# Optimization experiments

Hardware: AMD Instinct MI355X
Metric: run time of the kernel (lower is better)

The kernel has to match this reference:

```python
import jax, jax.numpy as jnp
import numpy as np

N = 50000
E = 800000
D = 128
NUM_GRAPHS = 64
NEG_SLOPE = 0.2


def _gat_conv(x, src, dst, W, a_src, a_dst, bias):
    """PyG GATConv with heads=1, concat=True. src/dst include self-loops."""
    h = x @ W                                  # [N, D_out]
    alpha_s = h @ a_src                        # [N]
    alpha_d = h @ a_dst                        # [N]
    e = alpha_s[src] + alpha_d[dst]            # [E_tot] edge scores
    e = jnp.where(e > 0, e, NEG_SLOPE * e)     # LeakyReLU(0.2)
    # numerically-stable softmax over incoming edges of each dst node
    m = jax.ops.segment_max(e, dst, num_segments=N)
    m = jnp.where(jnp.isfinite(m), m, 0.0)
    ex = jnp.exp(e - m[dst])
    s = jax.ops.segment_sum(ex, dst, num_segments=N)
    coef = ex / (s[dst] + 1e-16)               # [E_tot]
    msg = h[src] * coef[:, None]               # [E_tot, D_out] gathered messages
    out = jax.ops.segment_sum(msg, dst, num_segments=N)
    return out + bias


def setup_inputs() -> dict:
    key = jax.random.key(0)
    ks = jax.random.split(key, 12)
    x = jax.random.normal(ks[0], (N, D), dtype=jnp.float32)
    edge_index = jax.random.randint(ks[1], (2, E), 0, N, dtype=jnp.int64)
    batch = jnp.sort(jax.random.randint(ks[2], (N,), 0, NUM_GRAPHS, dtype=jnp.int64))
    g = 1.0 / np.sqrt(D)
    W1 = jax.random.normal(ks[3], (D, D), dtype=jnp.float32) * g
    as1 = jax.random.normal(ks[4], (D,), dtype=jnp.float32) * g
    ad1 = jax.random.normal(ks[5], (D,), dtype=jnp.float32) * g
    b1 = jnp.zeros((D,), dtype=jnp.float32)
    W2 = jax.random.normal(ks[6], (D, D), dtype=jnp.float32) * g
    as2 = jax.random.normal(ks[7], (D,), dtype=jnp.float32) * g
    ad2 = jax.random.normal(ks[8], (D,), dtype=jnp.float32) * g
    b2 = jnp.zeros((D,), dtype=jnp.float32)
    return {"x": x, "edge_index": edge_index, "batch": batch,
            "W1": W1, "as1": as1, "ad1": ad1, "b1": b1,
            "W2": W2, "as2": as2, "ad2": ad2, "b2": b2}


def reference(x, edge_index, batch, W1, as1, ad1, b1, W2, as2, ad2, b2):
    # PyG GATConv adds self-loops by default
    loops = jnp.arange(N, dtype=edge_index.dtype)
    src = jnp.concatenate([edge_index[0], loops])
    dst = jnp.concatenate([edge_index[1], loops])
    feats = _gat_conv(x, src, dst, W1, as1, ad1, b1)
    feats = _gat_conv(feats, src, dst, W2, as2, ad2, b2)
    # global mean pool over graphs in the batch
    sums = jax.ops.segment_sum(feats, batch, num_segments=NUM_GRAPHS)
    counts = jax.ops.segment_sum(jnp.ones((N,), feats.dtype), batch, num_segments=NUM_GRAPHS)
    pooled = sums / jnp.maximum(counts, 1.0)[:, None]
    return feats, pooled
```

## Files before the change

kernel.cpp:

```cpp
#include <hip/hip_runtime.h>

#define NN 50000
#define NE 800000
#define DIM 128
#define NG 64
#define ETOT (NE + NN)
#define NEG_SLOPE 0.2f
#define PB 200
#define MAXLG 8
#define NSH 8
#define SHW ((NN + NSH - 1) / NSH)
#define NB_SCAN ((NN + 255) / 256)

typedef unsigned int uint32;

static __device__ __forceinline__ uint32 f2bf_pack(float lo, float hi) {
  uint32 a = __float_as_uint(lo), b = __float_as_uint(hi);
  a = (a + 0x7fffu + ((a >> 16) & 1u)) >> 16;
  b = (b + 0x7fffu + ((b >> 16) & 1u)) >> 16;
  return a | (b << 16);
}
static __device__ __forceinline__ float bf_lo(uint32 u) { return __uint_as_float(u << 16); }
static __device__ __forceinline__ float bf_hi(uint32 u) { return __uint_as_float(u & 0xffff0000u); }


__global__ __launch_bounds__(256) void k_init(int* deg, int* fill, float* pooled, float* cnt) {
  int i = blockIdx.x * 256 + threadIdx.x;
  if (i < NN) { deg[i] = 1; fill[i] = 1; }
  if (i < NG * DIM) pooled[i] = 0.f;
  if (i < NG) cnt[i] = 0.f;
}

__global__ __launch_bounds__(256) void k_count(const int* __restrict__ dst, int* __restrict__ deg) {
  int e = blockIdx.x * 256 + threadIdx.x;
  if (e < NE) atomicAdd(&deg[dst[e]], 1);
}


__global__ __launch_bounds__(256) void k_scan1(const int* __restrict__ deg, int* __restrict__ offs,
                                               int* __restrict__ bsum) {
  __shared__ int ws[4];
  const int i = blockIdx.x * 256 + threadIdx.x;
  const int lane = threadIdx.x & 63, wid = threadIdx.x >> 6;
  int x = (i < NN) ? deg[i] : 0;
#pragma unroll
  for (int off = 1; off < 64; off <<= 1) {
    int t = __shfl_up(x, off, 64);
    if (lane >= off) x += t;
  }
  if (lane == 63) ws[wid] = x;
  __syncthreads();
  int pre = 0;
#pragma unroll
  for (int j = 0; j < 3; ++j) if (j < wid) pre += ws[j];
  x += pre;
  if (i < NN) offs[i + 1] = x;
  if (threadIdx.x == 255) bsum[blockIdx.x] = x;
}

__global__ __launch_bounds__(256) void k_scan2(const int* __restrict__ bsum, int* __restrict__ bpre) {
  __shared__ int ws[4];
  const int b = threadIdx.x;
  const int lane = b & 63, wid = b >> 6;
  int v = (b < NB_SCAN) ? bsum[b] : 0;
  int x = v;
#pragma unroll
  for (int off = 1; off < 64; off <<= 1) {
    int t = __shfl_up(x, off, 64);
    if (lane >= off) x += t;
  }
  if (lane == 63) ws[wid] = x;
  __syncthreads();
  int pre = 0;
#pragma unroll
  for (int j = 0; j < 3; ++j) if (j < wid) pre += ws[j];
  x += pre;
  if (b < NB_SCAN) bpre[b] = x - v;
}

__global__ __launch_bounds__(256) void k_scan3(int* __restrict__ offs, const int* __restrict__ bpre) {
  const int i = blockIdx.x * 256 + threadIdx.x;
  if (i < NN) offs[i + 1] += bpre[blockIdx.x];
  if (i == 0) offs[0] = 0;
}

__global__ __launch_bounds__(256) void k_selfloop(const int* __restrict__ offs, int* __restrict__ csr) {
  int i = blockIdx.x * 256 + threadIdx.x;
  if (i < NN) csr[offs[i]] = i;
}

__global__ __launch_bounds__(256) void k_scatter(const int* __restrict__ src, const int* __restrict__ dst,
                                                 const int* __restrict__ offs, int* __restrict__ fill,
                                                 int* __restrict__ csr) {
  const int r = blockIdx.x & (NSH - 1);
  const int bi = blockIdx.x >> 3;
  const int nb = gridDim.x >> 3;
  const int lo = r * SHW, hi = min(lo + SHW, NN);
  for (int e = bi * 256 + threadIdx.x; e < NE; e += nb * 256) {
    int d = dst[e];
    if (d >= lo && d < hi) {
      int p = offs[d] + atomicAdd(&fill[d], 1);
      csr[p] = src[e];
    }
  }
}


__global__ __launch_bounds__(256) void k_gemm(const float* __restrict__ X, const float* __restrict__ W,
                                              const float* __restrict__ a_s, const float* __restrict__ a_d,
                                              uint32* __restrict__ H16,
                                              float* __restrict__ alpha_s, float* __restrict__ alpha_d,
                                              int n) {
  __shared__ float sA[64][36];
  __shared__ float sB[32][132];
  const int tid = threadIdx.x;
  const int tx = tid & 15;
  const int ty = tid >> 4;
  const int row0 = blockIdx.x * 64;
  float acc[4][8];
#pragma unroll
  for (int i = 0; i < 4; ++i)
#pragma unroll
    for (int j = 0; j < 8; ++j) acc[i][j] = 0.f;

  for (int k0 = 0; k0 < DIM; k0 += 32) {
#pragma unroll
    for (int i = 0; i < 2; ++i) {
      int idx = tid + i * 256;
      int r = idx >> 3, c4 = idx & 7;
      int rg = row0 + r; if (rg > n - 1) rg = n - 1;
      float4 v = *(const float4*)(X + (size_t)rg * DIM + k0 + c4 * 4);
      *(float4*)&sA[r][c4 * 4] = v;
    }
#pragma unroll
    for (int i = 0; i < 4; ++i) {
      int idx = tid + i * 256;
      int k = idx >> 5, c4 = idx & 31;
      float4 v = *(const float4*)(W + (size_t)(k0 + k) * DIM + c4 * 4);
      *(float4*)&sB[k][c4 * 4] = v;
    }
    __syncthreads();
#pragma unroll 8
    for (int k = 0; k < 32; ++k) {
      float a[4], b[8];
#pragma unroll
      for (int i = 0; i < 4; ++i) a[i] = sA[ty * 4 + i][k];
      float4 b0 = *(const float4*)&sB[k][tx * 8];
      float4 b1 = *(const float4*)&sB[k][tx * 8 + 4];
      b[0] = b0.x; b[1] = b0.y; b[2] = b0.z; b[3] = b0.w;
      b[4] = b1.x; b[5] = b1.y; b[6] = b1.z; b[7] = b1.w;
#pragma unroll
      for (int i = 0; i < 4; ++i)
#pragma unroll
        for (int j = 0; j < 8; ++j) acc[i][j] = fmaf(a[i], b[j], acc[i][j]);
    }
    __syncthreads();
  }

  float4 s0 = *(const float4*)(a_s + tx * 8);
  float4 s1 = *(const float4*)(a_s + tx * 8 + 4);
  float4 d0 = *(const float4*)(a_d + tx * 8);
  float4 d1 = *(const float4*)(a_d + tx * 8 + 4);

#pragma unroll
  for (int i = 0; i < 4; ++i) {
    int r = row0 + ty * 4 + i;
    if (r < n) {
      uint4 pv = make_uint4(f2bf_pack(acc[i][0], acc[i][1]), f2bf_pack(acc[i][2], acc[i][3]),
                            f2bf_pack(acc[i][4], acc[i][5]), f2bf_pack(acc[i][6], acc[i][7]));
      *(uint4*)(H16 + (size_t)r * 64 + tx * 4) = pv;
    }
    float ps = acc[i][0] * s0.x + acc[i][1] * s0.y + acc[i][2] * s0.z + acc[i][3] * s0.w
             + acc[i][4] * s1.x + acc[i][5] * s1.y + acc[i][6] * s1.z + acc[i][7] * s1.w;
    float pd = acc[i][0] * d0.x + acc[i][1] * d0.y + acc[i][2] * d0.z + acc[i][3] * d0.w
             + acc[i][4] * d1.x + acc[i][5] * d1.y + acc[i][6] * d1.z + acc[i][7] * d1.w;
#pragma unroll
    for (int off = 1; off < 16; off <<= 1) {
      ps += __shfl_xor(ps, off, 64);
      pd += __shfl_xor(pd, off, 64);
    }
    if (tx == 0 && r < n) { alpha_s[r] = ps; alpha_d[r] = pd; }
  }
}


__global__ __launch_bounds__(256) void k_gemm16(const uint32* __restrict__ X16, const float* __restrict__ W,
                                                const float* __restrict__ a_s, const float* __restrict__ a_d,
                                                uint32* __restrict__ H16,
                                                float* __restrict__ alpha_s, float* __restrict__ alpha_d,
                                                int n) {
  __shared__ float sA[64][36];
  __shared__ float sB[32][132];
  const int tid = threadIdx.x;
  const int tx = tid & 15;
  const int ty = tid >> 4;
  const int row0 = blockIdx.x * 64;
  float acc[4][8];
#pragma unroll
  for (int i = 0; i < 4; ++i)
#pragma unroll
    for (int j = 0; j < 8; ++j) acc[i][j] = 0.f;

  for (int k0 = 0; k0 < DIM; k0 += 32) {
    {
      int r = tid >> 2, c = tid & 3;
      int rg = row0 + r; if (rg > n - 1) rg = n - 1;
      uint4 v = *(const uint4*)(X16 + (size_t)rg * 64 + (k0 >> 1) + c * 4);
      float* dst = &sA[r][c * 8];
      dst[0] = bf_lo(v.x); dst[1] = bf_hi(v.x);
      dst[2] = bf_lo(v.y); dst[3] = bf_hi(v.y);
      dst[4] = bf_lo(v.z); dst[5] = bf_hi(v.z);
      dst[6] = bf_lo(v.w); dst[7] = bf_hi(v.w);
    }
#pragma unroll
    for (int i = 0; i < 4; ++i) {
      int idx = tid + i * 256;
      int k = idx >> 5, c4 = idx & 31;
      float4 v = *(const float4*)(W + (size_t)(k0 + k) * DIM + c4 * 4);
      *(float4*)&sB[k][c4 * 4] = v;
    }
    __syncthreads();
#pragma unroll 8
    for (int k = 0; k < 32; ++k) {
      float a[4], b[8];
#pragma unroll
      for (int i = 0; i < 4; ++i) a[i] = sA[ty * 4 + i][k];
      float4 b0 = *(const float4*)&sB[k][tx * 8];
      float4 b1 = *(const float4*)&sB[k][tx * 8 + 4];
      b[0] = b0.x; b[1] = b0.y; b[2] = b0.z; b[3] = b0.w;
      b[4] = b1.x; b[5] = b1.y; b[6] = b1.z; b[7] = b1.w;
#pragma unroll
      for (int i = 0; i < 4; ++i)
#pragma unroll
        for (int j = 0; j < 8; ++j) acc[i][j] = fmaf(a[i], b[j], acc[i][j]);
    }
    __syncthreads();
  }

  float4 s0 = *(const float4*)(a_s + tx * 8);
  float4 s1 = *(const float4*)(a_s + tx * 8 + 4);
  float4 d0 = *(const float4*)(a_d + tx * 8);
  float4 d1 = *(const float4*)(a_d + tx * 8 + 4);

#pragma unroll
  for (int i = 0; i < 4; ++i) {
    int r = row0 + ty * 4 + i;
    if (r < n) {
      uint4 pv = make_uint4(f2bf_pack(acc[i][0], acc[i][1]), f2bf_pack(acc[i][2], acc[i][3]),
                            f2bf_pack(acc[i][4], acc[i][5]), f2bf_pack(acc[i][6], acc[i][7]));
      *(uint4*)(H16 + (size_t)r * 64 + tx * 4) = pv;
    }
    float ps = acc[i][0] * s0.x + acc[i][1] * s0.y + acc[i][2] * s0.z + acc[i][3] * s0.w
             + acc[i][4] * s1.x + acc[i][5] * s1.y + acc[i][6] * s1.z + acc[i][7] * s1.w;
    float pd = acc[i][0] * d0.x + acc[i][1] * d0.y + acc[i][2] * d0.z + acc[i][3] * d0.w
             + acc[i][4] * d1.x + acc[i][5] * d1.y + acc[i][6] * d1.z + acc[i][7] * d1.w;
#pragma unroll
    for (int off = 1; off < 16; off <<= 1) {
      ps += __shfl_xor(ps, off, 64);
      pd += __shfl_xor(pd, off, 64);
    }
    if (tx == 0 && r < n) { alpha_s[r] = ps; alpha_d[r] = pd; }
  }
}


#define AGGR4(J)                                                        \
  { int s0 = __shfl(sv, (J), 64), s1 = __shfl(sv, (J) + 1, 64),         \
        s2 = __shfl(sv, (J) + 2, 64), s3 = __shfl(sv, (J) + 3, 64);     \
    float c0 = __shfl(ex, (J), 64), c1 = __shfl(ex, (J) + 1, 64),       \
          c2 = __shfl(ex, (J) + 2, 64), c3 = __shfl(ex, (J) + 3, 64);   \
    uint32 u0 = H16[(size_t)s0 * 64 + l];                               \
    uint32 u1 = H16[(size_t)s1 * 64 + l];                               \
    uint32 u2 = H16[(size_t)s2 * 64 + l];                               \
    uint32 u3 = H16[(size_t)s3 * 64 + l];                               \
    ax = fmaf(c0, bf_lo(u0), ax); ay = fmaf(c0, bf_hi(u0), ay);         \
    ax = fmaf(c1, bf_lo(u1), ax); ay = fmaf(c1, bf_hi(u1), ay);         \
    ax = fmaf(c2, bf_lo(u2), ax); ay = fmaf(c2, bf_hi(u2), ay);         \
    ax = fmaf(c3, bf_lo(u3), ax); ay = fmaf(c3, bf_hi(u3), ay); }

#define AGGR1(J)                                                        \
  { int s0 = __shfl(sv, (J), 64); float c0 = __shfl(ex, (J), 64);       \
    uint32 u0 = H16[(size_t)s0 * 64 + l];                               \
    ax = fmaf(c0, bf_lo(u0), ax); ay = fmaf(c0, bf_hi(u0), ay); }

template <int STORE16>
__global__ __launch_bounds__(256) void k_sm_aggr(const int* __restrict__ offs, const int* __restrict__ csr,
                                                 const float* __restrict__ alpha_s, const float* __restrict__ alpha_d,
                                                 const uint32* __restrict__ H16, const float* __restrict__ bias,
                                                 float* __restrict__ out, uint32* __restrict__ out16) {
  const int wave = (blockIdx.x * 256 + threadIdx.x) >> 6;
  const int l = threadIdx.x & 63;
  if (wave >= NN) return;
  const int beg = offs[wave], end = offs[wave + 1];
  const int deg = end - beg;
  const float ad = alpha_d[wave];
  float ax = 0.f, ay = 0.f, ssum = 0.f;

  if (deg <= 64) {
    int sv = 0; float sc = -1e30f;
    if (l < deg) {
      sv = csr[beg + l];
      sc = alpha_s[sv] + ad;
      sc = sc > 0.f ? sc : NEG_SLOPE * sc;
    }
    float m = sc;
#pragma unroll
    for (int off = 1; off < 64; off <<= 1) m = fmaxf(m, __shfl_xor(m, off, 64));
    float ex = (l < deg) ? __expf(sc - m) : 0.f;
    ssum = ex;
    int j = 0;
    for (; j + 3 < deg; j += 4) AGGR4(j);
    for (; j < deg; ++j) AGGR1(j);
  } else {
    float m = -1e30f;
    for (int b = beg + l; b < end; b += 64) {
      float sc = alpha_s[csr[b]] + ad;
      sc = sc > 0.f ? sc : NEG_SLOPE * sc;
      m = fmaxf(m, sc);
    }
#pragma unroll
    for (int off = 1; off < 64; off <<= 1) m = fmaxf(m, __shfl_xor(m, off, 64));
    for (int base = beg; base < end; base += 64) {
      int nch = min(64, end - base);
      int sv = 0; float ex = 0.f;
      if (l < nch) {
        sv = csr[base + l];
        float sc = alpha_s[sv] + ad;
        sc = sc > 0.f ? sc : NEG_SLOPE * sc;
        ex = __expf(sc - m);
      }
      ssum += ex;
      int j = 0;
      for (; j + 3 < nch; j += 4) AGGR4(j);
      for (; j < nch; ++j) AGGR1(j);
    }
  }

#pragma unroll
  for (int off = 1; off < 64; off <<= 1) ssum += __shfl_xor(ssum, off, 64);
  const float inv = 1.f / (ssum + 1e-16f);
  float2 b = *(const float2*)(bias + 2 * l);
  float ox = ax * inv + b.x, oy = ay * inv + b.y;
  if (STORE16) {
    out16[(size_t)wave * 64 + l] = f2bf_pack(ox, oy);
  } else {
    *(float2*)(out + (size_t)wave * DIM + 2 * l) = make_float2(ox, oy);
  }
}


__global__ __launch_bounds__(256) void k_pool_partial(const float* __restrict__ feats,
                                                      const int* __restrict__ batch,
                                                      float* __restrict__ pooled, float* __restrict__ cnt) {
  __shared__ float acc[4][MAXLG][DIM];
  __shared__ float lcnt[4][MAXLG];
  const int tid = threadIdx.x;
  const int wid = tid >> 6, l = tid & 63;
  for (int i = tid; i < 4 * MAXLG * DIM; i += 256) ((float*)acc)[i] = 0.f;
  if (tid < 4 * MAXLG) ((float*)lcnt)[tid] = 0.f;
  __syncthreads();

  const int chunk = (NN + PB - 1) / PB;
  const int beg = blockIdx.x * chunk;
  const int end = min(beg + chunk, NN);
  const int g0 = (beg < NN) ? batch[beg] : 0;

  for (int node = beg + wid; node < end; node += 4) {
    int lg = batch[node] - g0;
    float2 v = *(const float2*)(feats + (size_t)node * DIM + 2 * l);
    if (lg < MAXLG) {
      acc[wid][lg][2 * l] += v.x;
      acc[wid][lg][2 * l + 1] += v.y;
      if (l == 0) lcnt[wid][lg] += 1.f;
    } else {
      atomicAdd(&pooled[(g0 + lg) * DIM + 2 * l], v.x);
      atomicAdd(&pooled[(g0 + lg) * DIM + 2 * l + 1], v.y);
      if (l == 0) atomicAdd(&cnt[g0 + lg], 1.f);
    }
  }
  __syncthreads();

  for (int i = tid; i < MAXLG * DIM; i += 256) {
    int lg = i >> 7, d = i & (DIM - 1);
    float s = acc[0][lg][d] + acc[1][lg][d] + acc[2][lg][d] + acc[3][lg][d];
    if (s != 0.f) atomicAdd(&pooled[(g0 + lg) * DIM + d], s);
  }
  if (tid < MAXLG) {
    float s = lcnt[0][tid] + lcnt[1][tid] + lcnt[2][tid] + lcnt[3][tid];
    if (s != 0.f) atomicAdd(&cnt[g0 + tid], s);
  }
}

__global__ __launch_bounds__(256) void k_pool_norm(float* pooled, const float* __restrict__ cnt) {
  int i = blockIdx.x * 256 + threadIdx.x;
  if (i < NG * DIM) pooled[i] /= fmaxf(cnt[i >> 7], 1.f);
}


static inline size_t pad256(size_t x) { return (x + 255) & ~(size_t)255; }

extern "C" void kernel_launch(void* const* d_in, const int* in_sizes, int n_in,
                              void* d_out, int out_size, void* d_ws, size_t ws_size,
                              hipStream_t stream) {
  const float* x   = (const float*)d_in[0];
  const int* ei    = (const int*)d_in[1];
  const int* batch = (const int*)d_in[2];
  const float* W1  = (const float*)d_in[3];
  const float* as1 = (const float*)d_in[4];
  const float* ad1 = (const float*)d_in[5];
  const float* b1  = (const float*)d_in[6];
  const float* W2  = (const float*)d_in[7];
  const float* as2 = (const float*)d_in[8];
  const float* ad2 = (const float*)d_in[9];
  const float* b2  = (const float*)d_in[10];

  float* out_feats = (float*)d_out;
  float* pooled    = out_feats + (size_t)NN * DIM;

  const int* src = ei;
  const int* dst = ei + NE;

  char* w = (char*)d_ws;
  uint32* h16 = (uint32*)w;   w += pad256((size_t)NN * 64 * 4);
  uint32* f116 = (uint32*)w;  w += pad256((size_t)NN * 64 * 4);
  float* alpha_s = (float*)w; w += pad256((size_t)NN * 4);
  float* alpha_d = (float*)w; w += pad256((size_t)NN * 4);
  int* deg  = (int*)w;        w += pad256((size_t)NN * 4);
  int* offs = (int*)w;        w += pad256((size_t)(NN + 1) * 4);
  int* fill = (int*)w;        w += pad256((size_t)NN * 4);
  int* csr  = (int*)w;        w += pad256((size_t)ETOT * 4);
  float* cnt  = (float*)w;    w += pad256((size_t)NG * 4);
  int* bsum = (int*)w;        w += pad256((size_t)NB_SCAN * 4);
  int* bpre = (int*)w;        w += pad256((size_t)NB_SCAN * 4);

  const int NB_N = (NN + 255) / 256;
  const int NB_E = (NE + 255) / 256;
  const int NB_W = (NN * 64 + 255) / 256;
  const int NB_G = (NN + 63) / 64;
  const int NB_SC = 1024;

  k_init<<<NB_N, 256, 0, stream>>>(deg, fill, pooled, cnt);
  k_count<<<NB_E, 256, 0, stream>>>(dst, deg);
  k_scan1<<<NB_SCAN, 256, 0, stream>>>(deg, offs, bsum);
  k_scan2<<<1, 256, 0, stream>>>(bsum, bpre);
  k_scan3<<<NB_SCAN, 256, 0, stream>>>(offs, bpre);
  k_selfloop<<<NB_N, 256, 0, stream>>>(offs, csr);
  k_scatter<<<NB_SC, 256, 0, stream>>>(src, dst, offs, fill, csr);

  k_gemm<<<NB_G, 256, 0, stream>>>(x, W1, as1, ad1, h16, alpha_s, alpha_d, NN);
  k_sm_aggr<1><<<NB_W, 256, 0, stream>>>(offs, csr, alpha_s, alpha_d, h16, b1, nullptr, f116);

  k_gemm16<<<NB_G, 256, 0, stream>>>(f116, W2, as2, ad2, h16, alpha_s, alpha_d, NN);
  k_sm_aggr<0><<<NB_W, 256, 0, stream>>>(offs, csr, alpha_s, alpha_d, h16, b2, out_feats, nullptr);

  k_pool_partial<<<PB, 256, 0, stream>>>(out_feats, batch, pooled, cnt);
  k_pool_norm<<<(NG * DIM + 255) / 256, 256, 0, stream>>>(pooled, cnt);
}
```

Baseline: 261.4 us.

## Replace FP32 SIMT GEMMs with bf16 MFMA GEMM using pre-transposed bf16 weights

Both dense projections now run through one templated kernel that uses 16x16x32 bf16 MFMA instructions in place of scalar FP32 FMAs. A small prep kernel transposes W1/W2 and converts them to bf16. Operands sit in XOR-swizzled shared memory, and the output is staged through LDS so the H16 stores are coalesced. The first layer's input x is now rounded to bf16 before the multiply, which loses some precision. The GEMMs are probably a modest share of total time next to the gather-heavy aggregation kernels.

```diff
diff --git a/kernel.cpp b/kernel.cpp
--- a/kernel.cpp
+++ b/kernel.cpp
@@ -13,6 +13,9 @@
 #define NB_SCAN ((NN + 255) / 256)
 
 typedef unsigned int uint32;
+typedef unsigned short ushort;
+typedef short bf16x8 __attribute__((ext_vector_type(8)));
+typedef float f32x4 __attribute__((ext_vector_type(4)));
 
 static __device__ __forceinline__ uint32 f2bf_pack(float lo, float hi) {
   uint32 a = __float_as_uint(lo), b = __float_as_uint(hi);
@@ -20,6 +23,11 @@
   b = (b + 0x7fffu + ((b >> 16) & 1u)) >> 16;
   return a | (b << 16);
 }
+static __device__ __forceinline__ ushort f2bf1(float x) {
+  uint32 a = __float_as_uint(x);
+  a = (a + 0x7fffu + ((a >> 16) & 1u)) >> 16;
+  return (ushort)a;
+}
 static __device__ __forceinline__ float bf_lo(uint32 u) { return __uint_as_float(u << 16); }
 static __device__ __forceinline__ float bf_hi(uint32 u) { return __uint_as_float(u & 0xffff0000u); }
 
@@ -29,6 +37,16 @@
   if (i < NN) { deg[i] = 1; fill[i] = 1; }
   if (i < NG * DIM) pooled[i] = 0.f;
   if (i < NG) cnt[i] = 0.f;
+}
+
+__global__ __launch_bounds__(256) void k_prep(const float* __restrict__ W1, const float* __restrict__ W2,
+                                              ushort* __restrict__ wt1, ushort* __restrict__ wt2) {
+  int i = blockIdx.x * 256 + threadIdx.x;
+  if (i < DIM * DIM) {
+    int n = i >> 7, k = i & 127;
+    wt1[i] = f2bf1(W1[k * DIM + n]);
+    wt2[i] = f2bf1(W2[k * DIM + n]);
+  }
 }
 
 __global__ __launch_bounds__(256) void k_count(const int* __restrict__ dst, int* __restrict__ deg) {
@@ -106,160 +124,103 @@
 }
 
 
-__global__ __launch_bounds__(256) void k_gemm(const float* __restrict__ X, const float* __restrict__ W,
-                                              const float* __restrict__ a_s, const float* __restrict__ a_d,
-                                              uint32* __restrict__ H16,
-                                              float* __restrict__ alpha_s, float* __restrict__ alpha_d,
-                                              int n) {
-  __shared__ float sA[64][36];
-  __shared__ float sB[32][132];
+template <int A16>
+__global__ __launch_bounds__(256) void k_mm(const void* __restrict__ Xv, const ushort* __restrict__ WT,
+                                            const float* __restrict__ a_s, const float* __restrict__ a_d,
+                                            uint32* __restrict__ H16,
+                                            float* __restrict__ alpha_s, float* __restrict__ alpha_d, int n) {
+  __shared__ __align__(16) ushort sWT[DIM * DIM];
+  __shared__ __align__(16) ushort sA[64 * DIM];
   const int tid = threadIdx.x;
-  const int tx = tid & 15;
-  const int ty = tid >> 4;
   const int row0 = blockIdx.x * 64;
-  float acc[4][8];
-#pragma unroll
-  for (int i = 0; i < 4; ++i)
-#pragma unroll
-    for (int j = 0; j < 8; ++j) acc[i][j] = 0.f;
-
-  for (int k0 = 0; k0 < DIM; k0 += 32) {
-#pragma unroll
-    for (int i = 0; i < 2; ++i) {
-      int idx = tid + i * 256;
-      int r = idx >> 3, c4 = idx & 7;
-      int rg = row0 + r; if (rg > n - 1) rg = n - 1;
-      float4 v = *(const float4*)(X + (size_t)rg * DIM + k0 + c4 * 4);
-      *(float4*)&sA[r][c4 * 4] = v;
-    }
-#pragma unroll
-    for (int i = 0; i < 4; ++i) {
-      int idx = tid + i * 256;
-      int k = idx >> 5, c4 = idx & 31;
-      float4 v = *(const float4*)(W + (size_t)(k0 + k) * DIM + c4 * 4);
-      *(float4*)&sB[k][c4 * 4] = v;
-    }
-    __syncthreads();
-#pragma unroll 8
-    for (int k = 0; k < 32; ++k) {
-      float a[4], b[8];
-#pragma unroll
-      for (int i = 0; i < 4; ++i) a[i] = sA[ty * 4 + i][k];
-      float4 b0 = *(const float4*)&sB[k][tx * 8];
-      float4 b1 = *(const float4*)&sB[k][tx * 8 + 4];
-      b[0] = b0.x; b[1] = b0.y; b[2] = b0.z; b[3] = b0.w;
-      b[4] = b1.x; b[5] = b1.y; b[6] = b1.z; b[7] = b1.w;
-#pragma unroll
-      for (int i = 0; i < 4; ++i)
-#pragma unroll
-        for (int j = 0; j < 8; ++j) acc[i][j] = fmaf(a[i], b[j], acc[i][j]);
-    }
-    __syncthreads();
-  }
-
-  float4 s0 = *(const float4*)(a_s + tx * 8);
-  float4 s1 = *(const float4*)(a_s + tx * 8 + 4);
-  float4 d0 = *(const float4*)(a_d + tx * 8);
-  float4 d1 = *(const float4*)(a_d + tx * 8 + 4);
-
-#pragma unroll
-  for (int i = 0; i < 4; ++i) {
-    int r = row0 + ty * 4 + i;
-    if (r < n) {
-      uint4 pv = make_uint4(f2bf_pack(acc[i][0], acc[i][1]), f2bf_pack(acc[i][2], acc[i][3]),
-                            f2bf_pack(acc[i][4], acc[i][5]), f2bf_pack(acc[i][6], acc[i][7]));
-      *(uint4*)(H16 + (size_t)r * 64 + tx * 4) = pv;
-    }
-    float ps = acc[i][0] * s0.x + acc[i][1] * s0.y + acc[i][2] * s0.z + acc[i][3] * s0.w
-             + acc[i][4] * s1.x + acc[i][5] * s1.y + acc[i][6] * s1.z + acc[i][7] * s1.w;
-    float pd = acc[i][0] * d0.x + acc[i][1] * d0.y + acc[i][2] * d0.z + acc[i][3] * d0.w
-             + acc[i][4] * d1.x + acc[i][5] * d1.y + acc[i][6] * d1.z + acc[i][7] * d1.w;
+
+  {
+    const int nr = tid >> 1, h2 = tid & 1;
+    const uint4* wp = (const uint4*)(WT + nr * DIM + h2 * 64);
+#pragma unroll
+    for (int i = 0; i < 8; ++i) {
+      uint4 v = wp[i];
+      int byte = nr * 256 + (((h2 * 128 + i * 16)) ^ ((nr & 7) << 4));
+      *(uint4*)((char*)sWT + byte) = v;
+    }
+  }
+  {
+    const int r = tid >> 2, q = tid & 3;
+    int rg = row0 + r; if (rg > n - 1) rg = n - 1;
+    if (A16) {
+      const uint4* xp = (const uint4*)((const uint32*)Xv + (size_t)rg * 64 + q * 16);
+#pragma unroll
+      for (int i = 0; i < 4; ++i) {
+        uint4 pk = xp[i];
+        int byte = r * 256 + ((q * 64 + i * 16) ^ ((r & 7) << 4));
+        *(uint4*)((char*)sA + byte) = pk;
+      }
+    } else {
+      const float4* xp = (const float4*)((const float*)Xv + (size_t)rg * DIM + q * 32);
+#pragma unroll
+      for (int i = 0; i < 4; ++i) {
+        float4 v0 = xp[2 * i], v1 = xp[2 * i + 1];
+        uint4 pk = make_uint4(f2bf_pack(v0.x, v0.y), f2bf_pack(v0.z, v0.w),
+                              f2bf_pack(v1.x, v1.y), f2bf_pack(v1.z, v1.w));
+        int byte = r * 256 + ((q * 64 + i * 16) ^ ((r & 7) << 4));
+        *(uint4*)((char*)sA + byte) = pk;
+      }
+    }
+  }
+  __syncthreads();
+
+  const int l = tid & 63, wv = tid >> 6;
+  const int jr = l & 15, g = l >> 4;
+  const int m0 = wv * 16;
+  f32x4 acc[8];
+#pragma unroll
+  for (int nt = 0; nt < 8; ++nt) acc[nt] = (f32x4){0.f, 0.f, 0.f, 0.f};
+
+  const int ra = m0 + jr;
+  const int abase = ra * 256, aswz = (ra & 7) << 4;
+  const int bswz = (jr & 7) << 4;
+#pragma unroll
+  for (int kk = 0; kk < 4; ++kk) {
+    const int kb = kk * 64 + g * 16;
+    bf16x8 af = *(const bf16x8*)((const char*)sA + abase + (kb ^ aswz));
+#pragma unroll
+    for (int nt = 0; nt < 8; ++nt) {
+      bf16x8 bfg = *(const bf16x8*)((const char*)sWT + (nt * 16 + jr) * 256 + (kb ^ bswz));
+      acc[nt] = __builtin_amdgcn_mfma_f32_16x16x32_bf16(af, bfg, acc[nt], 0, 0, 0);
+    }
+  }
+
+  float asv[8], adv[8];
+#pragma unroll
+  for (int nt = 0; nt < 8; ++nt) { asv[nt] = a_s[nt * 16 + jr]; adv[nt] = a_d[nt * 16 + jr]; }
+#pragma unroll
+  for (int j = 0; j < 4; ++j) {
+    float ps = 0.f, pd = 0.f;
+#pragma unroll
+    for (int nt = 0; nt < 8; ++nt) {
+      ps = fmaf(acc[nt][j], asv[nt], ps);
+      pd = fmaf(acc[nt][j], adv[nt], pd);
+    }
 #pragma unroll
     for (int off = 1; off < 16; off <<= 1) {
       ps += __shfl_xor(ps, off, 64);
       pd += __shfl_xor(pd, off, 64);
     }
-    if (tx == 0 && r < n) { alpha_s[r] = ps; alpha_d[r] = pd; }
-  }
-}
-
-
-__global__ __launch_bounds__(256) void k_gemm16(const uint32* __restrict__ X16, const float* __restrict__ W,
-                                                const float* __restrict__ a_s, const float* __restrict__ a_d,
-                                                uint32* __restrict__ H16,
-                                                float* __restrict__ alpha_s, float* __restrict__ alpha_d,
-                                                int n) {
-  __shared__ float sA[64][36];
-  __shared__ float sB[32][132];
-  const int tid = threadIdx.x;
-  const int tx = tid & 15;
-  const int ty = tid >> 4;
-  const int row0 = blockIdx.x * 64;
-  float acc[4][8];
-#pragma unroll
-  for (int i = 0; i < 4; ++i)
-#pragma unroll
-    for (int j = 0; j < 8; ++j) acc[i][j] = 0.f;
-
-  for (int k0 = 0; k0 < DIM; k0 += 32) {
-    {
-      int r = tid >> 2, c = tid & 3;
-      int rg = row0 + r; if (rg > n - 1) rg = n - 1;
-      uint4 v = *(const uint4*)(X16 + (size_t)rg * 64 + (k0 >> 1) + c * 4);
-      float* dst = &sA[r][c * 8];
-      dst[0] = bf_lo(v.x); dst[1] = bf_hi(v.x);
-      dst[2] = bf_lo(v.y); dst[3] = bf_hi(v.y);
-      dst[4] = bf_lo(v.z); dst[5] = bf_hi(v.z);
-      dst[6] = bf_lo(v.w); dst[7] = bf_hi(v.w);
-    }
-#pragma unroll
-    for (int i = 0; i < 4; ++i) {
-      int idx = tid + i * 256;
-      int k = idx >> 5, c4 = idx & 31;
-      float4 v = *(const float4*)(W + (size_t)(k0 + k) * DIM + c4 * 4);
-      *(float4*)&sB[k][c4 * 4] = v;
-    }
-    __syncthreads();
-#pragma unroll 8
-    for (int k = 0; k < 32; ++k) {
-      float a[4], b[8];
-#pragma unroll
-      for (int i = 0; i < 4; ++i) a[i] = sA[ty * 4 + i][k];
-      float4 b0 = *(const float4*)&sB[k][tx * 8];
-      float4 b1 = *(const float4*)&sB[k][tx * 8 + 4];
-      b[0] = b0.x; b[1] = b0.y; b[2] = b0.z; b[3] = b0.w;
-      b[4] = b1.x; b[5] = b1.y; b[6] = b1.z; b[7] = b1.w;
-#pragma unroll
-      for (int i = 0; i < 4; ++i)
-#pragma unroll
-        for (int j = 0; j < 8; ++j) acc[i][j] = fmaf(a[i], b[j], acc[i][j]);
-    }
-    __syncthreads();
-  }
-
-  float4 s0 = *(const float4*)(a_s + tx * 8);
-  float4 s1 = *(const float4*)(a_s + tx * 8 + 4);
-  float4 d0 = *(const float4*)(a_d + tx * 8);
-  float4 d1 = *(const float4*)(a_d + tx * 8 + 4);
-
+    int r = row0 + m0 + g * 4 + j;
+    if (jr == 0 && r < n) { alpha_s[r] = ps; alpha_d[r] = pd; }
+  }
+
+  ushort* sOut = sA;
+#pragma unroll
+  for (int nt = 0; nt < 8; ++nt)
+#pragma unroll
+    for (int j = 0; j < 4; ++j)
+      sOut[(m0 + g * 4 + j) * DIM + nt * 16 + jr] = f2bf1(acc[nt][j]);
 #pragma unroll
   for (int i = 0; i < 4; ++i) {
-    int r = row0 + ty * 4 + i;
-    if (r < n) {
-      uint4 pv = make_uint4(f2bf_pack(acc[i][0], acc[i][1]), f2bf_pack(acc[i][2], acc[i][3]),
-                            f2bf_pack(acc[i][4], acc[i][5]), f2bf_pack(acc[i][6], acc[i][7]));
-      *(uint4*)(H16 + (size_t)r * 64 + tx * 4) = pv;
-    }
-    float ps = acc[i][0] * s0.x + acc[i][1] * s0.y + acc[i][2] * s0.z + acc[i][3] * s0.w
-             + acc[i][4] * s1.x + acc[i][5] * s1.y + acc[i][6] * s1.z + acc[i][7] * s1.w;
-    float pd = acc[i][0] * d0.x + acc[i][1] * d0.y + acc[i][2] * d0.z + acc[i][3] * d0.w
-             + acc[i][4] * d1.x + acc[i][5] * d1.y + acc[i][6] * d1.z + acc[i][7] * d1.w;
-#pragma unroll
-    for (int off = 1; off < 16; off <<= 1) {
-      ps += __shfl_xor(ps, off, 64);
-      pd += __shfl_xor(pd, off, 64);
-    }
-    if (tx == 0 && r < n) { alpha_s[r] = ps; alpha_d[r] = pd; }
+    int r = row0 + m0 + (l >> 4) + i * 4;
+    uint4 v = *(const uint4*)((const char*)sOut + m0 * 256 + l * 16 + i * 1024);
+    if (r < n) *(uint4*)(H16 + (size_t)(row0 + m0) * 64 + l * 4 + i * 256) = v;
   }
 }
 
@@ -432,6 +393,8 @@
   float* cnt  = (float*)w;    w += pad256((size_t)NG * 4);
   int* bsum = (int*)w;        w += pad256((size_t)NB_SCAN * 4);
   int* bpre = (int*)w;        w += pad256((size_t)NB_SCAN * 4);
+  ushort* wt1 = (ushort*)w;   w += pad256((size_t)DIM * DIM * 2);
+  ushort* wt2 = (ushort*)w;   w += pad256((size_t)DIM * DIM * 2);
 
   const int NB_N = (NN + 255) / 256;
   const int NB_E = (NE + 255) / 256;
@@ -440,6 +403,7 @@
   const int NB_SC = 1024;
 
   k_init<<<NB_N, 256, 0, stream>>>(deg, fill, pooled, cnt);
+  k_prep<<<(DIM * DIM + 255) / 256, 256, 0, stream>>>(W1, W2, wt1, wt2);
   k_count<<<NB_E, 256, 0, stream>>>(dst, deg);
   k_scan1<<<NB_SCAN, 256, 0, stream>>>(deg, offs, bsum);
   k_scan2<<<1, 256, 0, stream>>>(bsum, bpre);
@@ -447,10 +411,10 @@
   k_selfloop<<<NB_N, 256, 0, stream>>>(offs, csr);
   k_scatter<<<NB_SC, 256, 0, stream>>>(src, dst, offs, fill, csr);
 
-  k_gemm<<<NB_G, 256, 0, stream>>>(x, W1, as1, ad1, h16, alpha_s, alpha_d, NN);
+  k_mm<0><<<NB_G, 256, 0, stream>>>(x, wt1, as1, ad1, h16, alpha_s, alpha_d, NN);
   k_sm_aggr<1><<<NB_W, 256, 0, stream>>>(offs, csr, alpha_s, alpha_d, h16, b1, nullptr, f116);
 
-  k_gemm16<<<NB_G, 256, 0, stream>>>(f116, W2, as2, ad2, h16, alpha_s, alpha_d, NN);
+  k_mm<1><<<NB_G, 256, 0, stream>>>(f116, wt2, as2, ad2, h16, alpha_s, alpha_d, NN);
   k_sm_aggr<0><<<NB_W, 256, 0, stream>>>(offs, csr, alpha_s, alpha_d, h16, b2, out_feats, nullptr);
 
   k_pool_partial<<<PB, 256, 0, stream>>>(out_feats, batch, pooled, cnt);
```

Result: faster. 222.9 us (-14.7%).
